# Optimization experiments

Measured on AMD Instinct MI355X. Metric: run time of the kernel, lower is better.

## Reference

```python
import jax, jax.numpy as jnp
import numpy as np
from jax import lax


def setup_inputs() -> dict:
    key = jax.random.key(0)
    ks = jax.random.split(key, 9)
    B, Hh, Ww, Cin, Cout, F, E = 8, 64, 64, 256, 256, 128, 256
    s = 0.02  # glorot-ish scale to keep the H->pow(-0.5) chain numerically sane
    return {
        "x": jax.random.normal(ks[0], (B, Hh, Ww, Cin), jnp.float32),
        "w_phi": jax.random.normal(ks[1], (Cin, F), jnp.float32) * s,
        "b_phi": jnp.zeros((F,), jnp.float32),
        "w_a": jax.random.normal(ks[2], (Cin, F), jnp.float32) * s,
        "b_a": jnp.zeros((F,), jnp.float32),
        "w_m": jax.random.normal(ks[3], (7, 7, Cin, E), jnp.float32) * s,
        "b_m": jnp.zeros((E,), jnp.float32),
        "weight_2": jax.random.normal(ks[4], (Cin, Cout), jnp.float32) * s,
        "bias_2": jnp.zeros((Cout,), jnp.float32),
    }


def reference(x, w_phi, b_phi, w_a, b_a, w_m, b_m, weight_2, bias_2):
    B, Hh, Ww, Cin = x.shape
    V = Hh * Ww
    F = w_phi.shape[1]
    E = w_m.shape[-1]

    # phi: 1x1 conv -> [B, V, F]
    phi = (jnp.einsum('bhwc,cf->bhwf', x, w_phi) + b_phi).reshape(B, V, F)

    # A: global average pool + 1x1 conv -> diagonal scale vector [B, F]
    a = jnp.mean(x, axis=(1, 2)) @ w_a + b_a  # (B, F)

    # M: 7x7 SAME conv -> [B, V, E]
    M = lax.conv_general_dilated(
        x, w_m, window_strides=(1, 1), padding='SAME',
        dimension_numbers=('NHWC', 'HWIO', 'NHWC')) + b_m
    M = M.reshape(B, V, E)

    # H = |phi @ diag(a) @ phi^T @ M| without materializing diag(a)
    t = jnp.einsum('bvf,bve->bfe', phi, M)        # phi^T @ M : (B, F, E)
    t = a[:, :, None] * t                          # diag(a) scaling
    Hmat = jnp.abs(jnp.einsum('bvf,bfe->bve', phi, t))  # (B, V, E)

    D = jnp.sum(Hmat, axis=2)                      # vertex degree (B, V)
    D_H = D[:, :, None] ** -0.5 * Hmat             # D^{-1/2} H
    Binv = 1.0 / jnp.sum(Hmat, axis=1)             # edge degree inverse (B, E)

    feats = x.reshape(B, V, Cin)
    tmp = jnp.einsum('bve,bvc->bec', D_H, feats)   # D_H^T @ features
    tmp = Binv[:, :, None] * tmp                   # diag(B^{-1}) scaling
    agg = jnp.einsum('bve,bec->bvc', D_H, tmp)     # D_H @ ...

    out = (feats - agg) @ weight_2 + bias_2        # (B, V, Cout)
    return out.reshape(B, Hh, Ww, -1)
```

## Files before the change

kernel.cpp:

```cpp
#include <hip/hip_runtime.h>
#include <hip/hip_bf16.h>

typedef unsigned short u16;
typedef unsigned int u32;
#define DI __device__ __forceinline__

typedef __attribute__((ext_vector_type(8))) short v8s;
typedef __attribute__((ext_vector_type(4))) float v4f;

constexpr int B_ = 8;
constexpr int V_ = 4096;
constexpr int C_ = 256;
constexpr int F_ = 128;
constexpr int E_ = 256;
constexpr int KK_ = 49;
constexpr int PWS = 80;
constexpr int PS  = 5600;

constexpr size_t OFF_XSUM   = 0;
constexpr size_t OFF_CSUM   = 2048;
constexpr size_t OFF_SPHI   = 4096;
constexpr size_t OFF_A      = 5120;
constexpr size_t OFF_T      = 6144;
constexpr size_t OFF_TMPT   = 268288;
constexpr size_t ZERO_HEAD  = 792576;
constexpr size_t OFF_TT16   = 792576;
constexpr size_t OFF_T2T16  = 923648;
constexpr size_t OFF_W2T16  = 1185792;
constexpr size_t OFF_PHIT   = 1218560;
constexpr size_t OFF_XPT    = 3315712;
constexpr size_t XPT_FLOATS = 5734400;
constexpr size_t OFF_WMT    = 9050112;

DI float bf2f(u16 u) {
    union { u32 i; float f; } v; v.i = ((u32)u) << 16; return v.f;
}
DI u16 f2bf(float f) {
    union { float f; u32 i; } v; v.f = f;
    u32 r = v.i + 0x7fff + ((v.i >> 16) & 1);
    return (u16)(r >> 16);
}

__global__ void k_xsum(const float* __restrict__ x, float* __restrict__ ws) {
    int b = blockIdx.x >> 3;
    int chunk = blockIdx.x & 7;
    int c = threadIdx.x;
    const float* xb = x + ((size_t)b * V_ + chunk * 512) * C_ + c;
    float s = 0.f;
    for (int v = 0; v < 512; ++v) s += xb[(size_t)v * C_];
    atomicAdd(&ws[OFF_XSUM + b * C_ + c], s);
}

__global__ void k_a(const float* __restrict__ w_a, const float* __restrict__ b_a,
                    float* __restrict__ ws) {
    int b = blockIdx.x, f = threadIdx.x;
    float acc = b_a[f];
    const float* xs = &ws[OFF_XSUM + b * C_];
    for (int c = 0; c < C_; ++c)
        acc += (xs[c] * (1.0f / 4096.0f)) * w_a[c * F_ + f];
    ws[OFF_A + b * F_ + f] = acc;
}

__global__ void k_phi(const float* __restrict__ x, const float* __restrict__ w_phi,
                      const float* __restrict__ b_phi, float* __restrict__ ws) {
    __shared__ float xsT[C_][8];
    int r0 = blockIdx.x * 8;
    int b = r0 >> 12;
    int v0 = r0 & 4095;
    int tid = threadIdx.x;
    const float* xb = x + (size_t)r0 * C_;
    for (int i = tid; i < 8 * C_; i += 128) xsT[i & 255][i >> 8] = xb[i];
    __syncthreads();
    int f = tid;
    float bp = b_phi[f];
    float acc[8];
#pragma unroll
    for (int r = 0; r < 8; ++r) acc[r] = bp;
    const float* wp = w_phi + f;
    for (int c = 0; c < C_; ++c) {
        float w = wp[c * F_];
        float4 xa = *(const float4*)&xsT[c][0];
        float4 xb4 = *(const float4*)&xsT[c][4];
        acc[0] += xa.x * w;  acc[1] += xa.y * w;  acc[2] += xa.z * w;  acc[3] += xa.w * w;
        acc[4] += xb4.x * w; acc[5] += xb4.y * w; acc[6] += xb4.z * w; acc[7] += xb4.w * w;
    }
    u16 pb[8];
    float ssum = 0.f;
#pragma unroll
    for (int r = 0; r < 8; ++r) { pb[r] = f2bf(acc[r]); ssum += acc[r]; }
    u16* phiT = (u16*)&ws[OFF_PHIT];
    uint4 q;
    q.x = (u32)pb[0] | ((u32)pb[1] << 16);
    q.y = (u32)pb[2] | ((u32)pb[3] << 16);
    q.z = (u32)pb[4] | ((u32)pb[5] << 16);
    q.w = (u32)pb[6] | ((u32)pb[7] << 16);
    *(uint4*)(phiT + ((size_t)(b * F_ + f)) * V_ + v0) = q;
    atomicAdd(&ws[OFF_SPHI + b * F_ + f], ssum);
}

__global__ void k_padx(const float* __restrict__ x, float* __restrict__ ws) {
    __shared__ float tile[64][68];
    int b = blockIdx.x >> 6;
    int h = blockIdx.x & 63;
    int tid = threadIdx.x;
    u16* xpt = (u16*)&ws[OFF_XPT];
    for (int cc = 0; cc < 4; ++cc) {
        int c0 = cc * 64;
        int w = tid >> 2, q = tid & 3;
        const float* xr = x + ((size_t)(b * V_ + h * 64 + w)) * C_ + c0 + q * 16;
        float4 f0 = *(const float4*)(xr);
        float4 f1 = *(const float4*)(xr + 4);
        float4 f2 = *(const float4*)(xr + 8);
        float4 f3 = *(const float4*)(xr + 12);
        __syncthreads();
        *(float4*)&tile[w][q * 16]      = f0;
        *(float4*)&tile[w][q * 16 + 4]  = f1;
        *(float4*)&tile[w][q * 16 + 8]  = f2;
        *(float4*)&tile[w][q * 16 + 12] = f3;
        __syncthreads();
        int c = tid >> 2, j4 = tid & 3;
        u16* dst = xpt + ((size_t)(b * C_ + c0 + c)) * PS + (h + 3) * PWS + 3 + j4 * 16;
#pragma unroll
        for (int ww = 0; ww < 16; ++ww) dst[ww] = f2bf(tile[j4 * 16 + ww][c]);
    }
}

__global__ void k_wmt(const float* __restrict__ w_m, float* __restrict__ ws) {
    int kk = blockIdx.x;
    int e = threadIdx.x;
    u16* wmt = (u16*)&ws[OFF_WMT];
    for (int c0 = 0; c0 < C_; c0 += 8) {
        u16 pk[8];
#pragma unroll
        for (int i = 0; i < 8; ++i)
            pk[i] = f2bf(w_m[((size_t)kk * C_ + c0 + i) * E_ + e]);
        uint4 q;
        q.x = (u32)pk[0] | ((u32)pk[1] << 16);
        q.y = (u32)pk[2] | ((u32)pk[3] << 16);
        q.z = (u32)pk[4] | ((u32)pk[5] << 16);
        q.w = (u32)pk[6] | ((u32)pk[7] << 16);
        *(uint4*)(wmt + ((size_t)(kk * E_ + e)) * C_ + c0) = q;
    }
}

__global__ void k_w2t(const float* __restrict__ w2, float* __restrict__ ws) {
    int co = blockIdx.x, c = threadIdx.x;
    ((u16*)&ws[OFF_W2T16])[(size_t)co * C_ + c] = f2bf(w2[(size_t)c * C_ + co]);
}

template <int KX>
DI void g1_loop(const u16* __restrict__ phiT_b, const u16* __restrict__ xpt_b,
                int ky, u16* lds_a, u16* lds_b, int tid, v4f acc[4][4]) {
    int wave = tid >> 6, lane = tid & 63, quad = lane >> 4, l15 = lane & 15;
    int mi2 = wave >> 2, ni2 = wave & 3;
    int fA = tid >> 2, vsA = (tid & 3) * 8;
    int cB = tid >> 1, sB = (tid & 1) * 16;
    const u16* bbase = xpt_b + (size_t)cB * PS + (size_t)ky * PWS + sB;
    constexpr int J0 = KX >> 1;
#pragma unroll 1
    for (int chunk = 0; chunk < 128; ++chunk) {
        int v0 = chunk * 32;
        int h = chunk >> 1, w0 = (chunk & 1) * 32;
        uint4 a4 = *(const uint4*)(phiT_b + (size_t)fA * V_ + v0 + vsA);
        const u16* bp = bbase + h * PWS + w0;
        uint4 q0 = *(const uint4*)(bp);
        uint4 q1 = *(const uint4*)(bp + 8);
        u32 dw[12];
        dw[0] = q0.x; dw[1] = q0.y; dw[2] = q0.z; dw[3] = q0.w;
        dw[4] = q1.x; dw[5] = q1.y; dw[6] = q1.z; dw[7] = q1.w;
        if constexpr (KX >= 1) {
            uint4 q2 = *(const uint4*)(bp + 16);
            dw[8] = q2.x; dw[9] = q2.y; dw[10] = q2.z; dw[11] = q2.w;
        } else {
            dw[8] = dw[9] = dw[10] = dw[11] = 0;
        }
        u32 o[8];
        if constexpr ((KX & 1) == 0) {
#pragma unroll
            for (int i = 0; i < 8; ++i) o[i] = dw[J0 + i];
        } else {
#pragma unroll
            for (int i = 0; i < 8; ++i) o[i] = (dw[J0 + i] >> 16) | (dw[J0 + i + 1] << 16);
        }
        u16* la = lds_a + (chunk & 1) * (128 * 40);
        u16* lb = lds_b + (chunk & 1) * (256 * 40);
        *(uint4*)&la[fA * 40 + vsA] = a4;
        *(uint4*)&lb[cB * 40 + sB]     = (uint4){o[0], o[1], o[2], o[3]};
        *(uint4*)&lb[cB * 40 + sB + 8] = (uint4){o[4], o[5], o[6], o[7]};
        __syncthreads();
        v8s afr[4], bfr[4];
#pragma unroll
        for (int ai = 0; ai < 4; ++ai)
            afr[ai] = *(const v8s*)&la[(mi2 * 64 + ai * 16 + l15) * 40 + quad * 8];
#pragma unroll
        for (int bi = 0; bi < 4; ++bi)
            bfr[bi] = *(const v8s*)&lb[(ni2 * 64 + bi * 16 + l15) * 40 + quad * 8];
#pragma unroll
        for (int ai = 0; ai < 4; ++ai)
#pragma unroll
            for (int bi = 0; bi < 4; ++bi)
                acc[ai][bi] = __builtin_amdgcn_mfma_f32_16x16x32_bf16(
                    afr[ai], bfr[bi], acc[ai][bi], 0, 0, 0);
    }
}

__global__ __launch_bounds__(512, 2) void k_gemm1(const float* __restrict__ ws_c,
                                                  u16* __restrict__ G) {
    __shared__ u16 lds_a[2 * 128 * 40];
    __shared__ u16 lds_b[2 * 256 * 40];
    int b  = blockIdx.x & 7;
    int kk = blockIdx.x >> 3;
    int ky = kk / 7, kx = kk % 7;
    int tid = threadIdx.x;
    int wave = tid >> 6, lane = tid & 63, quad = lane >> 4, l15 = lane & 15;
    int mi2 = wave >> 2, ni2 = wave & 3;
    const u16* phiT_b = (const u16*)&ws_c[OFF_PHIT] + (size_t)b * F_ * V_;
    const u16* xpt_b  = (const u16*)&ws_c[OFF_XPT] + (size_t)b * C_ * PS;
    v4f acc[4][4];
#pragma unroll
    for (int i = 0; i < 4; ++i)
#pragma unroll
        for (int j = 0; j < 4; ++j) acc[i][j] = (v4f){0.f, 0.f, 0.f, 0.f};
    switch (kx) {
        case 0: g1_loop<0>(phiT_b, xpt_b, ky, lds_a, lds_b, tid, acc); break;
        case 1: g1_loop<1>(phiT_b, xpt_b, ky, lds_a, lds_b, tid, acc); break;
        case 2: g1_loop<2>(phiT_b, xpt_b, ky, lds_a, lds_b, tid, acc); break;
        case 3: g1_loop<3>(phiT_b, xpt_b, ky, lds_a, lds_b, tid, acc); break;
        case 4: g1_loop<4>(phiT_b, xpt_b, ky, lds_a, lds_b, tid, acc); break;
        case 5: g1_loop<5>(phiT_b, xpt_b, ky, lds_a, lds_b, tid, acc); break;
        case 6: g1_loop<6>(phiT_b, xpt_b, ky, lds_a, lds_b, tid, acc); break;
    }
    u16* Gb = G + ((size_t)(b * KK_ + kk)) * F_ * C_;
#pragma unroll
    for (int ai = 0; ai < 4; ++ai)
#pragma unroll
        for (int bi = 0; bi < 4; ++bi) {
            int c = ni2 * 64 + bi * 16 + l15;
#pragma unroll
            for (int r = 0; r < 4; ++r) {
                int f = mi2 * 64 + ai * 16 + quad * 4 + r;
                Gb[(size_t)f * C_ + c] = f2bf(acc[ai][bi][r]);
            }
        }
}

__global__ void k_gemm2(const u16* __restrict__ G, float* __restrict__ ws) {
    int blk = blockIdx.x;
    int kg = blk % 7; blk /= 7;
    int ei = blk % 4; blk /= 4;
    int fi = blk % 2; int b = blk / 2;
    int tid = threadIdx.x;
    int wave = tid >> 6, lane = tid & 63, quad = lane >> 4, l15 = lane & 15;
    int fbase = fi * 64 + wave * 16;
    int ebase = ei * 64;
    const u16* wmt = (const u16*)&ws[OFF_WMT];
    const u16* Gb = G + (size_t)b * KK_ * F_ * C_;
    v4f acc[4];
#pragma unroll
    for (int i = 0; i < 4; ++i) acc[i] = (v4f){0.f, 0.f, 0.f, 0.f};
    for (int kk = kg * 7; kk < kg * 7 + 7; ++kk) {
        const u16* Ga = Gb + ((size_t)kk * F_ + fbase + l15) * C_;
        const u16* Wb = wmt + ((size_t)kk * E_ + ebase + l15) * C_;
#pragma unroll 2
        for (int cs = 0; cs < 8; ++cs) {
            v8s af = *(const v8s*)(Ga + cs * 32 + quad * 8);
#pragma unroll
            for (int nt = 0; nt < 4; ++nt) {
                v8s bf = *(const v8s*)(Wb + (size_t)nt * 16 * C_ + cs * 32 + quad * 8);
                acc[nt] = __builtin_amdgcn_mfma_f32_16x16x32_bf16(af, bf, acc[nt], 0, 0, 0);
            }
        }
    }
#pragma unroll
    for (int nt = 0; nt < 4; ++nt)
#pragma unroll
        for (int r = 0; r < 4; ++r) {
            int e = ebase + nt * 16 + l15;
            int f = fbase + quad * 4 + r;
            atomicAdd(&ws[OFF_T + ((size_t)(b * E_ + e)) * F_ + f], acc[nt][r]);
        }
}

__global__ void k_tfix(const float* __restrict__ b_m, float* __restrict__ ws) {
    int b = blockIdx.x >> 8, e = blockIdx.x & 255, f = threadIdx.x;
    float av = ws[OFF_A + b * F_ + f];
    float sp = ws[OFF_SPHI + b * F_ + f];
    float t = av * (ws[OFF_T + ((size_t)(b * E_ + e)) * F_ + f] + sp * b_m[e]);
    ((u16*)&ws[OFF_TT16])[((size_t)(b * E_ + e)) * F_ + f] = f2bf(t);
}

__global__ void k_hd(float* __restrict__ ws) {
    __shared__ u16 phiL[64 * 136];
    __shared__ float cspart[4][E_];
    int b = blockIdx.x >> 6;
    int chunkIdx = blockIdx.x & 63;
    int v0 = chunkIdx * 64;
    int tid = threadIdx.x;
    {
        int f = tid & 127, seg = (tid >> 7) * 32;
        const u16* src = (const u16*)&ws[OFF_PHIT] + ((size_t)(b * F_ + f)) * V_ + v0 + seg;
        uint4 q0 = *(const uint4*)(src);
        uint4 q1 = *(const uint4*)(src + 8);
        uint4 q2 = *(const uint4*)(src + 16);
        uint4 q3 = *(const uint4*)(src + 24);
        u32 dw[16] = {q0.x, q0.y, q0.z, q0.w, q1.x, q1.y, q1.z, q1.w,
                      q2.x, q2.y, q2.z, q2.w, q3.x, q3.y, q3.z, q3.w};
#pragma unroll
        for (int j = 0; j < 16; ++j) {
            phiL[(seg + 2 * j) * 136 + f]     = (u16)(dw[j] & 0xffff);
            phiL[(seg + 2 * j + 1) * 136 + f] = (u16)(dw[j] >> 16);
        }
    }
    __syncthreads();
    int wave = tid >> 6, lane = tid & 63, quad = lane >> 4, l15 = lane & 15;
    const u16* tt = (const u16*)&ws[OFF_TT16] + (size_t)b * E_ * F_;
    v4f acc[16];
#pragma unroll
    for (int i = 0; i < 16; ++i) acc[i] = (v4f){0.f, 0.f, 0.f, 0.f};
#pragma unroll
    for (int kc = 0; kc < 4; ++kc) {
        v8s af = *(const v8s*)&phiL[(wave * 16 + l15) * 136 + kc * 32 + quad * 8];
#pragma unroll
        for (int nt = 0; nt < 16; ++nt) {
            v8s bf = *(const v8s*)(tt + (size_t)(nt * 16 + l15) * F_ + kc * 32 + quad * 8);
            acc[nt] = __builtin_amdgcn_mfma_f32_16x16x32_bf16(af, bf, acc[nt], 0, 0, 0);
        }
    }
#pragma unroll
    for (int nt = 0; nt < 16; ++nt)
#pragma unroll
        for (int r = 0; r < 4; ++r) acc[nt][r] = fabsf(acc[nt][r]);
    v4f rs = acc[0];
#pragma unroll
    for (int nt = 1; nt < 16; ++nt) rs += acc[nt];
#pragma unroll
    for (int m = 1; m < 16; m <<= 1) {
#pragma unroll
        for (int r = 0; r < 4; ++r) rs[r] += __shfl_xor(rs[r], m, 64);
    }
    float rsd[4];
#pragma unroll
    for (int r = 0; r < 4; ++r) rsd[r] = rsqrtf(rs[r]);
#pragma unroll
    for (int nt = 0; nt < 16; ++nt) {
        float cs = acc[nt][0] + acc[nt][1] + acc[nt][2] + acc[nt][3];
        cs += __shfl_xor(cs, 16, 64);
        cs += __shfl_xor(cs, 32, 64);
        if (quad == 0) cspart[wave][nt * 16 + l15] = cs;
    }
    u16* hm = (u16*)&ws[OFF_XPT];
#pragma unroll
    for (int nt = 0; nt < 16; ++nt)
#pragma unroll
        for (int r = 0; r < 4; ++r) {
            int v = v0 + wave * 16 + quad * 4 + r;
            hm[((size_t)(b * V_ + v)) * E_ + nt * 16 + l15] = f2bf(acc[nt][r] * rsd[r]);
        }
    __syncthreads();
    {
        int e = tid;
        float s = cspart[0][e] + cspart[1][e] + cspart[2][e] + cspart[3][e];
        ws[OFF_T + ((size_t)(b * 64 + chunkIdx)) * E_ + e] = s;
    }
}

__global__ void k_csum(float* __restrict__ ws) {
    int b = blockIdx.x, e = threadIdx.x;
    const float* p = &ws[OFF_T + (size_t)b * 64 * E_ + e];
    float s = 0.f;
    for (int i = 0; i < 64; ++i) s += p[(size_t)i * E_];
    ws[OFF_CSUM + b * E_ + e] = s;
}

__global__ __launch_bounds__(512, 2) void k_tmp(const float* __restrict__ x,
                                                float* __restrict__ ws) {
    __shared__ u16 xT[256 * 40];
    __shared__ u16 hT[128 * 40];
    int blk = blockIdx.x;
    int eh = blk & 1; blk >>= 1;
    int vs = blk & 15; int b = blk >> 4;
    int v0b = vs * 256;
    int tid = threadIdx.x;
    int wave = tid >> 6, lane = tid & 63, quad = lane >> 4, l15 = lane & 15;
    int m0 = wave * 32;
    const u16* hmS = (const u16*)&ws[OFF_XPT];
    v4f acc[2][8];
#pragma unroll
    for (int i = 0; i < 2; ++i)
#pragma unroll
        for (int j = 0; j < 8; ++j) acc[i][j] = (v4f){0.f, 0.f, 0.f, 0.f};
    int sv = tid & 31, sg = tid >> 5;
#pragma unroll 1
    for (int ch = 0; ch < 8; ++ch) {
        int vbase = v0b + ch * 32;
        const float* xr = x + ((size_t)(b * V_ + vbase + sv)) * C_ + sg * 16;
        float4 xf0 = *(const float4*)(xr);
        float4 xf1 = *(const float4*)(xr + 4);
        float4 xf2 = *(const float4*)(xr + 8);
        float4 xf3 = *(const float4*)(xr + 12);
        const u16* hr = hmS + ((size_t)(b * V_ + vbase + sv)) * E_ + eh * 128 + sg * 8;
        uint4 hq = *(const uint4*)hr;
        u16 hp[8] = {(u16)(hq.x & 0xffff), (u16)(hq.x >> 16), (u16)(hq.y & 0xffff),
                     (u16)(hq.y >> 16), (u16)(hq.z & 0xffff), (u16)(hq.z >> 16),
                     (u16)(hq.w & 0xffff), (u16)(hq.w >> 16)};
        float xv[16] = {xf0.x, xf0.y, xf0.z, xf0.w, xf1.x, xf1.y, xf1.z, xf1.w,
                        xf2.x, xf2.y, xf2.z, xf2.w, xf3.x, xf3.y, xf3.z, xf3.w};
        __syncthreads();
#pragma unroll
        for (int i = 0; i < 16; ++i) xT[(sg * 16 + i) * 40 + sv] = f2bf(xv[i]);
#pragma unroll
        for (int i = 0; i < 8; ++i) hT[(sg * 8 + i) * 40 + sv] = hp[i];
        __syncthreads();
        v8s a0 = *(const v8s*)&xT[(m0 + l15) * 40 + quad * 8];
        v8s a1 = *(const v8s*)&xT[(m0 + 16 + l15) * 40 + quad * 8];
#pragma unroll
        for (int nt = 0; nt < 8; ++nt) {
            v8s bf = *(const v8s*)&hT[(nt * 16 + l15) * 40 + quad * 8];
            acc[0][nt] = __builtin_amdgcn_mfma_f32_16x16x32_bf16(a0, bf, acc[0][nt], 0, 0, 0);
            acc[1][nt] = __builtin_amdgcn_mfma_f32_16x16x32_bf16(a1, bf, acc[1][nt], 0, 0, 0);
        }
    }
#pragma unroll
    for (int mt = 0; mt < 2; ++mt)
#pragma unroll
        for (int nt = 0; nt < 8; ++nt)
#pragma unroll
            for (int r = 0; r < 4; ++r) {
                int c = m0 + mt * 16 + quad * 4 + r;
                int e = eh * 128 + nt * 16 + l15;
                atomicAdd(&ws[OFF_TMPT + ((size_t)(b * C_ + c)) * E_ + e], acc[mt][nt][r]);
            }
}

__global__ void k_t2fix(float* __restrict__ ws) {
    int b = blockIdx.x >> 8, c = blockIdx.x & 255, e = threadIdx.x;
    float binv = 1.0f / ws[OFF_CSUM + b * E_ + e];
    float tv = ws[OFF_TMPT + ((size_t)(b * C_ + c)) * E_ + e];
    ((u16*)&ws[OFF_T2T16])[((size_t)(b * C_ + c)) * E_ + e] = f2bf(tv * binv);
}

__global__ __launch_bounds__(256, 2) void k_out(const float* __restrict__ x,
                                                const float* __restrict__ b2,
                                                const float* __restrict__ ws,
                                                float* __restrict__ io) {
    __shared__ u16 dL[64 * 264];
    int b = blockIdx.x >> 6;
    int v0 = (blockIdx.x & 63) * 64;
    int tid = threadIdx.x;
    int wave = tid >> 6, lane = tid & 63, quad = lane >> 4, l15 = lane & 15;
    const u16* hm = (const u16*)&ws[OFF_XPT] + ((size_t)(b * V_ + v0 + wave * 16 + l15)) * E_;
    const u16* t2 = (const u16*)&ws[OFF_T2T16] + (size_t)b * C_ * E_;
    v4f acc[16];
#pragma unroll
    for (int i = 0; i < 16; ++i) acc[i] = (v4f){0.f, 0.f, 0.f, 0.f};
#pragma unroll 2
    for (int kc = 0; kc < 8; ++kc) {
        v8s af = *(const v8s*)(hm + kc * 32 + quad * 8);
#pragma unroll
        for (int nt = 0; nt < 16; ++nt) {
            v8s bf = *(const v8s*)(t2 + (size_t)(nt * 16 + l15) * E_ + kc * 32 + quad * 8);
            acc[nt] = __builtin_amdgcn_mfma_f32_16x16x32_bf16(af, bf, acc[nt], 0, 0, 0);
        }
    }
#pragma unroll
    for (int nt = 0; nt < 16; ++nt)
#pragma unroll
        for (int r = 0; r < 4; ++r) {
            int v = wave * 16 + quad * 4 + r;
            int c = nt * 16 + l15;
            float xv = x[((size_t)(b * V_ + v0 + v)) * C_ + c];
            dL[v * 264 + c] = f2bf(xv - acc[nt][r]);
        }
    __syncthreads();
    const u16* w2t = (const u16*)&ws[OFF_W2T16];
    v4f acc2[16];
#pragma unroll
    for (int i = 0; i < 16; ++i) acc2[i] = (v4f){0.f, 0.f, 0.f, 0.f};
#pragma unroll 2
    for (int kc = 0; kc < 8; ++kc) {
        v8s af = *(const v8s*)&dL[(wave * 16 + l15) * 264 + kc * 32 + quad * 8];
#pragma unroll
        for (int nt = 0; nt < 16; ++nt) {
            v8s bf = *(const v8s*)(w2t + (size_t)(nt * 16 + l15) * C_ + kc * 32 + quad * 8);
            acc2[nt] = __builtin_amdgcn_mfma_f32_16x16x32_bf16(af, bf, acc2[nt], 0, 0, 0);
        }
    }
#pragma unroll
    for (int nt = 0; nt < 16; ++nt)
#pragma unroll
        for (int r = 0; r < 4; ++r) {
            int v = wave * 16 + quad * 4 + r;
            int co = nt * 16 + l15;
            io[((size_t)(b * V_ + v0 + v)) * C_ + co] = acc2[nt][r] + b2[co];
        }
}

extern "C" void kernel_launch(void* const* d_in, const int* in_sizes, int n_in,
                              void* d_out, int out_size, void* d_ws, size_t ws_size,
                              hipStream_t stream) {
    const float* x     = (const float*)d_in[0];
    const float* w_phi = (const float*)d_in[1];
    const float* b_phi = (const float*)d_in[2];
    const float* w_a   = (const float*)d_in[3];
    const float* b_a   = (const float*)d_in[4];
    const float* w_m   = (const float*)d_in[5];
    const float* b_m   = (const float*)d_in[6];
    const float* w2    = (const float*)d_in[7];
    const float* b2    = (const float*)d_in[8];
    float* ws = (float*)d_ws;
    float* io = (float*)d_out;

    hipMemsetAsync(ws, 0, ZERO_HEAD * sizeof(float), stream);
    hipMemsetAsync(ws + OFF_XPT, 0, XPT_FLOATS * sizeof(float), stream);
    k_xsum<<<dim3(64), dim3(256), 0, stream>>>(x, ws);
    k_a<<<dim3(8), dim3(128), 0, stream>>>(w_a, b_a, ws);
    k_phi<<<dim3(4096), dim3(128), 0, stream>>>(x, w_phi, b_phi, ws);
    k_padx<<<dim3(512), dim3(256), 0, stream>>>(x, ws);
    k_wmt<<<dim3(49), dim3(256), 0, stream>>>(w_m, ws);
    k_w2t<<<dim3(256), dim3(256), 0, stream>>>(w2, ws);
    k_gemm1<<<dim3(392), dim3(512), 0, stream>>>(ws, (u16*)d_out);
    k_gemm2<<<dim3(448), dim3(256), 0, stream>>>((const u16*)d_out, ws);
    k_tfix<<<dim3(2048), dim3(128), 0, stream>>>(b_m, ws);
    k_hd<<<dim3(512), dim3(256), 0, stream>>>(ws);
    k_csum<<<dim3(8), dim3(256), 0, stream>>>(ws);
    k_tmp<<<dim3(256), dim3(512), 0, stream>>>(x, ws);
    k_t2fix<<<dim3(2048), dim3(256), 0, stream>>>(ws);
    k_out<<<dim3(512), dim3(256), 0, stream>>>(x, b2, ws, io);
}
```

Before: 603.5 us.

## Load phi fragments directly, split xsum finer, replace tmp atomics with partial slices

```diff
diff --git a/kernel.cpp b/kernel.cpp
--- a/kernel.cpp
+++ b/kernel.cpp
@@ -16,6 +16,7 @@
 constexpr int KK_ = 49;
 constexpr int PWS = 80;
 constexpr int PS  = 5600;
+constexpr int SLICE = 524288;
 
 constexpr size_t OFF_XSUM   = 0;
 constexpr size_t OFF_CSUM   = 2048;
@@ -42,12 +43,12 @@
 }
 
 __global__ void k_xsum(const float* __restrict__ x, float* __restrict__ ws) {
-    int b = blockIdx.x >> 3;
-    int chunk = blockIdx.x & 7;
+    int b = blockIdx.x >> 5;
+    int chunk = blockIdx.x & 31;
     int c = threadIdx.x;
-    const float* xb = x + ((size_t)b * V_ + chunk * 512) * C_ + c;
+    const float* xb = x + ((size_t)b * V_ + chunk * 128) * C_ + c;
     float s = 0.f;
-    for (int v = 0; v < 512; ++v) s += xb[(size_t)v * C_];
+    for (int v = 0; v < 128; ++v) s += xb[(size_t)v * C_];
     atomicAdd(&ws[OFF_XSUM + b * C_ + c], s);
 }
 
@@ -150,18 +151,21 @@
 
 template <int KX>
 DI void g1_loop(const u16* __restrict__ phiT_b, const u16* __restrict__ xpt_b,
-                int ky, u16* lds_a, u16* lds_b, int tid, v4f acc[4][4]) {
+                int ky, u16* lds_b, int tid, v4f acc[4][4]) {
     int wave = tid >> 6, lane = tid & 63, quad = lane >> 4, l15 = lane & 15;
     int mi2 = wave >> 2, ni2 = wave & 3;
-    int fA = tid >> 2, vsA = (tid & 3) * 8;
     int cB = tid >> 1, sB = (tid & 1) * 16;
     const u16* bbase = xpt_b + (size_t)cB * PS + (size_t)ky * PWS + sB;
+    const u16* pA = phiT_b + (size_t)(mi2 * 64 + l15) * V_ + quad * 8;
     constexpr int J0 = KX >> 1;
 #pragma unroll 1
     for (int chunk = 0; chunk < 128; ++chunk) {
         int v0 = chunk * 32;
         int h = chunk >> 1, w0 = (chunk & 1) * 32;
-        uint4 a4 = *(const uint4*)(phiT_b + (size_t)fA * V_ + v0 + vsA);
+        v8s afr[4];
+#pragma unroll
+        for (int ai = 0; ai < 4; ++ai)
+            afr[ai] = *(const v8s*)(pA + (size_t)(ai * 16) * V_ + v0);
         const u16* bp = bbase + h * PWS + w0;
         uint4 q0 = *(const uint4*)(bp);
         uint4 q1 = *(const uint4*)(bp + 8);
@@ -182,16 +186,11 @@
 #pragma unroll
             for (int i = 0; i < 8; ++i) o[i] = (dw[J0 + i] >> 16) | (dw[J0 + i + 1] << 16);
         }
-        u16* la = lds_a + (chunk & 1) * (128 * 40);
         u16* lb = lds_b + (chunk & 1) * (256 * 40);
-        *(uint4*)&la[fA * 40 + vsA] = a4;
         *(uint4*)&lb[cB * 40 + sB]     = (uint4){o[0], o[1], o[2], o[3]};
         *(uint4*)&lb[cB * 40 + sB + 8] = (uint4){o[4], o[5], o[6], o[7]};
         __syncthreads();
-        v8s afr[4], bfr[4];
-#pragma unroll
-        for (int ai = 0; ai < 4; ++ai)
-            afr[ai] = *(const v8s*)&la[(mi2 * 64 + ai * 16 + l15) * 40 + quad * 8];
+        v8s bfr[4];
 #pragma unroll
         for (int bi = 0; bi < 4; ++bi)
             bfr[bi] = *(const v8s*)&lb[(ni2 * 64 + bi * 16 + l15) * 40 + quad * 8];
@@ -206,7 +205,6 @@
 
 __global__ __launch_bounds__(512, 2) void k_gemm1(const float* __restrict__ ws_c,
                                                   u16* __restrict__ G) {
-    __shared__ u16 lds_a[2 * 128 * 40];
     __shared__ u16 lds_b[2 * 256 * 40];
     int b  = blockIdx.x & 7;
     int kk = blockIdx.x >> 3;
@@ -222,13 +220,13 @@
 #pragma unroll
         for (int j = 0; j < 4; ++j) acc[i][j] = (v4f){0.f, 0.f, 0.f, 0.f};
     switch (kx) {
-        case 0: g1_loop<0>(phiT_b, xpt_b, ky, lds_a, lds_b, tid, acc); break;
-        case 1: g1_loop<1>(phiT_b, xpt_b, ky, lds_a, lds_b, tid, acc); break;
-        case 2: g1_loop<2>(phiT_b, xpt_b, ky, lds_a, lds_b, tid, acc); break;
-        case 3: g1_loop<3>(phiT_b, xpt_b, ky, lds_a, lds_b, tid, acc); break;
-        case 4: g1_loop<4>(phiT_b, xpt_b, ky, lds_a, lds_b, tid, acc); break;
-        case 5: g1_loop<5>(phiT_b, xpt_b, ky, lds_a, lds_b, tid, acc); break;
-        case 6: g1_loop<6>(phiT_b, xpt_b, ky, lds_a, lds_b, tid, acc); break;
+        case 0: g1_loop<0>(phiT_b, xpt_b, ky, lds_b, tid, acc); break;
+        case 1: g1_loop<1>(phiT_b, xpt_b, ky, lds_b, tid, acc); break;
+        case 2: g1_loop<2>(phiT_b, xpt_b, ky, lds_b, tid, acc); break;
+        case 3: g1_loop<3>(phiT_b, xpt_b, ky, lds_b, tid, acc); break;
+        case 4: g1_loop<4>(phiT_b, xpt_b, ky, lds_b, tid, acc); break;
+        case 5: g1_loop<5>(phiT_b, xpt_b, ky, lds_b, tid, acc); break;
+        case 6: g1_loop<6>(phiT_b, xpt_b, ky, lds_b, tid, acc); break;
     }
     u16* Gb = G + ((size_t)(b * KK_ + kk)) * F_ * C_;
 #pragma unroll
@@ -373,7 +371,8 @@
 }
 
 __global__ __launch_bounds__(512, 2) void k_tmp(const float* __restrict__ x,
-                                                float* __restrict__ ws) {
+                                                float* __restrict__ ws,
+                                                float* __restrict__ part) {
     __shared__ u16 xT[256 * 40];
     __shared__ u16 hT[128 * 40];
     int blk = blockIdx.x;
@@ -420,6 +419,7 @@
             acc[1][nt] = __builtin_amdgcn_mfma_f32_16x16x32_bf16(a1, bf, acc[1][nt], 0, 0, 0);
         }
     }
+    float* po = part + (size_t)vs * SLICE;
 #pragma unroll
     for (int mt = 0; mt < 2; ++mt)
 #pragma unroll
@@ -428,15 +428,18 @@
             for (int r = 0; r < 4; ++r) {
                 int c = m0 + mt * 16 + quad * 4 + r;
                 int e = eh * 128 + nt * 16 + l15;
-                atomicAdd(&ws[OFF_TMPT + ((size_t)(b * C_ + c)) * E_ + e], acc[mt][nt][r]);
+                po[((size_t)(b * C_ + c)) * E_ + e] = acc[mt][nt][r];
             }
 }
 
-__global__ void k_t2fix(float* __restrict__ ws) {
+__global__ void k_t2fix(const float* __restrict__ part, float* __restrict__ ws) {
     int b = blockIdx.x >> 8, c = blockIdx.x & 255, e = threadIdx.x;
     float binv = 1.0f / ws[OFF_CSUM + b * E_ + e];
-    float tv = ws[OFF_TMPT + ((size_t)(b * C_ + c)) * E_ + e];
-    ((u16*)&ws[OFF_T2T16])[((size_t)(b * C_ + c)) * E_ + e] = f2bf(tv * binv);
+    size_t idx = ((size_t)(b * C_ + c)) * E_ + e;
+    float tv = 0.f;
+#pragma unroll
+    for (int s = 0; s < 16; ++s) tv += part[(size_t)s * SLICE + idx];
+    ((u16*)&ws[OFF_T2T16])[idx] = f2bf(tv * binv);
 }
 
 __global__ __launch_bounds__(256, 2) void k_out(const float* __restrict__ x,
@@ -512,7 +515,7 @@
 
     hipMemsetAsync(ws, 0, ZERO_HEAD * sizeof(float), stream);
     hipMemsetAsync(ws + OFF_XPT, 0, XPT_FLOATS * sizeof(float), stream);
-    k_xsum<<<dim3(64), dim3(256), 0, stream>>>(x, ws);
+    k_xsum<<<dim3(256), dim3(256), 0, stream>>>(x, ws);
     k_a<<<dim3(8), dim3(128), 0, stream>>>(w_a, b_a, ws);
     k_phi<<<dim3(4096), dim3(128), 0, stream>>>(x, w_phi, b_phi, ws);
     k_padx<<<dim3(512), dim3(256), 0, stream>>>(x, ws);
@@ -523,7 +526,7 @@
     k_tfix<<<dim3(2048), dim3(128), 0, stream>>>(b_m, ws);
     k_hd<<<dim3(512), dim3(256), 0, stream>>>(ws);
     k_csum<<<dim3(8), dim3(256), 0, stream>>>(ws);
-    k_tmp<<<dim3(256), dim3(512), 0, stream>>>(x, ws);
-    k_t2fix<<<dim3(2048), dim3(256), 0, stream>>>(ws);
+    k_tmp<<<dim3(256), dim3(512), 0, stream>>>(x, ws, (float*)d_out);
+    k_t2fix<<<dim3(2048), dim3(256), 0, stream>>>((const float*)d_out, ws);
     k_out<<<dim3(512), dim3(256), 0, stream>>>(x, b2, ws, io);
 }
```

Result: slower. 733.4 us (+21.5%).
